# Kernel tuning notes

Measured on AMD Instinct MI355X. Metric: run time of the kernel, lower is better.

## Reference

```python
import jax, jax.numpy as jnp
import numpy as np

DIM = 1024
NUM_HEADS = 16


def setup_inputs() -> dict:
    key = jax.random.key(0)
    ks = jax.random.split(key, 7)
    B, N, C = 2, 2048, DIM
    s = 1.0 / np.sqrt(C)
    x = jax.random.normal(ks[0], (B, N, C), dtype=jnp.float32)
    Wq = jax.random.normal(ks[1], (C, C), dtype=jnp.float32) * s
    Wk = jax.random.normal(ks[2], (C, C), dtype=jnp.float32) * s
    Wv = jax.random.normal(ks[3], (C, C), dtype=jnp.float32) * s
    bq = jnp.zeros((C,), dtype=jnp.float32)
    bk = jnp.zeros((C,), dtype=jnp.float32)
    bv = jnp.zeros((C,), dtype=jnp.float32)
    return {"x": x, "Wq": Wq, "bq": bq, "Wk": Wk, "bk": bk, "Wv": Wv, "bv": bv}


def reference(x, Wq, bq, Wk, bk, Wv, bv):
    B, N, C = x.shape
    H = NUM_HEADS
    D = C // H
    # Linear projections (torch Linear: x @ W.T + b)
    q = (x @ Wq.T + bq).reshape(B, N, H, D).transpose(0, 2, 1, 3)  # [B,H,N,D]
    k = (x @ Wk.T + bk).reshape(B, N, H, D).transpose(0, 2, 1, 3)
    v = (x @ Wv.T + bv).reshape(B, N, H, D).transpose(0, 2, 1, 3)
    # NOTE: original scales by sqrt(dim)=sqrt(C), not sqrt(head_dim)
    scale = 1.0 / np.sqrt(C).astype(np.float32)
    logits = jnp.einsum('bhnd,bhmd->bhnm', q, k) * scale  # [B,H,N,N]
    attn = jax.nn.softmax(logits, axis=-1)
    out = jnp.einsum('bhnm,bhmd->bhnd', attn, v)  # [B,H,N,D]
    return out.transpose(0, 2, 1, 3).reshape(B, N, C)
```

## Files before the change

### kernel.cpp

```cpp
#include <hip/hip_runtime.h>

typedef __attribute__((ext_vector_type(8))) short bf16x8;
typedef __attribute__((ext_vector_type(4))) float f32x4;
typedef __attribute__((ext_vector_type(16))) float f32x16;
typedef __attribute__((ext_vector_type(8))) unsigned short us8;
typedef unsigned short u16;
typedef unsigned int u32;

__device__ inline u16 f2bf(float f) {
  union { float f; unsigned u; } v; v.f = f;
  unsigned r = v.u + 0x7FFFu + ((v.u >> 16) & 1u);
  return (u16)(r >> 16);
}

__device__ inline u32 cvtpk_bf16(float lo, float hi) {
  u32 r;
  asm volatile("v_cvt_pk_bf16_f32 %0, %1, %2" : "=v"(r) : "v"(lo), "v"(hi));
  return r;
}

__device__ inline void gload_lds16(const void* g, void* l) {
  __builtin_amdgcn_global_load_lds(
      (const __attribute__((address_space(1))) void*)g,
      (__attribute__((address_space(3))) void*)l, 16, 0, 0);
}

__global__ void cvt_all(const float* __restrict__ x, const float* __restrict__ wq,
                        const float* __restrict__ wk, const float* __restrict__ wv,
                        u16* __restrict__ out) {
  int i = (blockIdx.x * blockDim.x + threadIdx.x) * 4;
  const float* src; int off;
  if (i < 4194304)      { src = x;  off = 0; }
  else if (i < 5242880) { src = wq; off = 4194304; }
  else if (i < 6291456) { src = wk; off = 5242880; }
  else                  { src = wv; off = 6291456; }
  float4 v = *reinterpret_cast<const float4*>(src + (i - off));
  ushort4 o;
  o.x = f2bf(v.x); o.y = f2bf(v.y); o.z = f2bf(v.z); o.w = f2bf(v.w);
  *reinterpret_cast<ushort4*>(out + i) = o;
}

__global__ __launch_bounds__(256, 3) void gemm_qkv(
    const u16* __restrict__ X,
    const u16* __restrict__ Wq, const u16* __restrict__ Wk, const u16* __restrict__ Wv,
    const float* __restrict__ bq, const float* __restrict__ bk, const float* __restrict__ bv,
    u16* __restrict__ Oq, u16* __restrict__ Ok, u16* __restrict__ Ov)
{
  constexpr int GK = 1024;
  __shared__ __align__(16) u16 As[128 * 64];
  __shared__ __align__(16) u16 Bs[128 * 64];

  const int z = blockIdx.z;
  const u16* W = (z == 0) ? Wq : (z == 1) ? Wk : Wv;
  const float* bias = (z == 0) ? bq : (z == 1) ? bk : bv;
  u16* O = (z == 0) ? Oq : (z == 1) ? Ok : Ov;
  const float scale = (z == 0) ? (1.4426950408889634f / 32.0f) : 1.0f;

  const int tid = threadIdx.x;
  const int lane = tid & 63, w = tid >> 6;
  const int wm = w >> 1, wn = w & 1;
  const int q = lane & 15, g = lane >> 4;
  const int bm0 = blockIdx.x * 128, bn0 = blockIdx.y * 128;

  int srow[4], sgc[4];
  #pragma unroll
  for (int i = 0; i < 4; ++i) {
    int c = i * 256 + tid;
    srow[i] = c >> 3;
    sgc[i] = (((c & 7) ^ ((c >> 3) & 7)) * 8);
  }

  f32x4 acc[4][4];
  #pragma unroll
  for (int i = 0; i < 4; ++i)
    #pragma unroll
    for (int j = 0; j < 4; ++j) acc[i][j] = (f32x4){0.f, 0.f, 0.f, 0.f};

  for (int k0 = 0; k0 < GK; k0 += 64) {
    #pragma unroll
    for (int i = 0; i < 4; ++i) {
      int c8 = (i * 256 + tid) * 8;
      gload_lds16(&X[(bm0 + srow[i]) * GK + k0 + sgc[i]], &As[c8]);
      gload_lds16(&W[(bn0 + srow[i]) * GK + k0 + sgc[i]], &Bs[c8]);
    }
    __syncthreads();

    #pragma unroll
    for (int kk = 0; kk < 2; ++kk) {
      bf16x8 af[4], bfr[4];
      #pragma unroll
      for (int mi = 0; mi < 4; ++mi) {
        int row = wm * 64 + mi * 16 + q;
        af[mi] = *reinterpret_cast<const bf16x8*>(
            &As[row * 64 + (((kk * 4 + g) ^ (row & 7)) * 8)]);
      }
      #pragma unroll
      for (int ni = 0; ni < 4; ++ni) {
        int row = wn * 64 + ni * 16 + q;
        bfr[ni] = *reinterpret_cast<const bf16x8*>(
            &Bs[row * 64 + (((kk * 4 + g) ^ (row & 7)) * 8)]);
      }
      #pragma unroll
      for (int mi = 0; mi < 4; ++mi)
        #pragma unroll
        for (int ni = 0; ni < 4; ++ni)
          acc[mi][ni] = __builtin_amdgcn_mfma_f32_16x16x32_bf16(af[mi], bfr[ni], acc[mi][ni], 0, 0, 0);
    }
    __syncthreads();
  }

  #pragma unroll
  for (int mi = 0; mi < 4; ++mi) {
    #pragma unroll
    for (int ni = 0; ni < 4; ++ni) {
      int col = bn0 + wn * 64 + ni * 16 + q;
      float bb = bias[col];
      int h = col >> 6, d = col & 63;
      #pragma unroll
      for (int r = 0; r < 4; ++r) {
        int row = bm0 + wm * 64 + mi * 16 + 4 * g + r;
        int b = row >> 11, n = row & 2047;
        float v = (acc[mi][ni][r] + bb) * scale;
        O[(((b << 4) + h) * 2048 + n) * 64 + d] = f2bf(v);
      }
    }
  }
}

__global__ __launch_bounds__(512, 4) void attn_kernel(
    const u16* __restrict__ Q, const u16* __restrict__ K, const u16* __restrict__ V,
    float* __restrict__ out)
{
  __shared__ __align__(16) u16 smem[32768];
  u16* Kbase = smem;
  u16* Vbase = smem + 16384;

  const int tid = threadIdx.x;
  const int lane = tid & 63, w = tid >> 6;
  const int half = w >> 2, w4 = w & 3;
  const int tid256 = w4 * 64 + lane;
  const int ql = lane & 31, h = lane >> 5, l7 = lane & 7;

  const int lin = blockIdx.x;
  const int xcd = lin & 7, li = lin >> 3;
  const int bh = xcd * 4 + (li >> 4);
  const int b = bh >> 4, hd = bh & 15;
  const int qrow0 = (li & 15) * 128 + w4 * 32;

  const u16* Qp = Q + (bh * 2048 + qrow0 + ql) * 64;
  const u16* Kp = K + (bh * 2048 + half * 1024) * 64;
  const u16* Vp = V + (bh * 2048 + half * 1024) * 64;

  bf16x8 qf[4];
  #pragma unroll
  for (int ks = 0; ks < 4; ++ks)
    qf[ks] = *reinterpret_cast<const bf16x8*>(Qp + 16 * ks + 8 * h);

  int krow_i[2], kcolb_i[2];
  #pragma unroll
  for (int i = 0; i < 2; ++i) {
    int c = i * 256 + tid256;
    krow_i[i] = c >> 3;
    kcolb_i[i] = 16 * ((c & 7) ^ ((c >> 3) & 7));
  }

  f32x16 o0, o1;
  #pragma unroll
  for (int i = 0; i < 16; ++i) { o0[i] = 0.0f; o1[i] = 0.0f; }
  float lsum = 0.0f;

  u16* Kh = Kbase + half * 8192;
  u16* Vh = Vbase + half * 8192;
  char* vwb = (char*)(Vh) + w4 * 1024;
  const int l2 = lane * 2;

  {
    #pragma unroll
    for (int i = 0; i < 2; ++i)
      gload_lds16((const char*)(Kp + krow_i[i] * 64) + kcolb_i[i],
                  &Kh[i * 2048 + w4 * 512]);
    us8 v0 = *reinterpret_cast<const us8*>(Vp + lane * 64 + 8 * w4);
    us8 v1 = *reinterpret_cast<const us8*>(Vp + lane * 64 + 8 * (w4 + 4));
    #pragma unroll
    for (int i = 0; i < 8; ++i) {
      *(u16*)(vwb + ((i * 144) ^ l2)) = v0[i];
      *(u16*)(vwb + 4096 + ((i * 144) ^ l2)) = v1[i];
    }
    __syncthreads();
  }

  us8 vreg0, vreg1;
  for (int t = 0; t < 16; ++t) {
    const int cur = t & 1, nxt = cur ^ 1;
    const int kb = t * 64;
    if (t < 15) {
      #pragma unroll
      for (int i = 0; i < 2; ++i)
        gload_lds16((const char*)(Kp + (kb + 64 + krow_i[i]) * 64) + kcolb_i[i],
                    &Kh[nxt * 4096 + i * 2048 + w4 * 512]);
      vreg0 = *reinterpret_cast<const us8*>(Vp + (kb + 64 + lane) * 64 + 8 * w4);
      vreg1 = *reinterpret_cast<const us8*>(Vp + (kb + 64 + lane) * 64 + 8 * (w4 + 4));
    }

    f32x16 p0, p1;
    #pragma unroll
    for (int i = 0; i < 16; ++i) { p0[i] = 0.0f; p1[i] = 0.0f; }
    const u16* kl = Kh + cur * 4096;
    __builtin_amdgcn_s_setprio(1);
    #pragma unroll
    for (int ks = 0; ks < 4; ++ks) {
      int cb = (16 * ks + 8 * h) ^ (l7 << 3);
      bf16x8 kf0 = *reinterpret_cast<const bf16x8*>(kl + ql * 64 + cb);
      p0 = __builtin_amdgcn_mfma_f32_32x32x16_bf16(kf0, qf[ks], p0, 0, 0, 0);
      bf16x8 kf1 = *reinterpret_cast<const bf16x8*>(kl + (32 + ql) * 64 + cb);
      p1 = __builtin_amdgcn_mfma_f32_32x32x16_bf16(kf1, qf[ks], p1, 0, 0, 0);
    }
    __builtin_amdgcn_s_setprio(0);

    #pragma unroll
    for (int i = 0; i < 16; ++i) {
      p0[i] = __builtin_amdgcn_exp2f(p0[i]);
      p1[i] = __builtin_amdgcn_exp2f(p1[i]);
    }
    float sa[8];
    #pragma unroll
    for (int i = 0; i < 8; ++i)
      sa[i] = (p0[i] + p0[i + 8]) + (p1[i] + p1[i + 8]);
    float rs = ((sa[0] + sa[1]) + (sa[2] + sa[3])) + ((sa[4] + sa[5]) + (sa[6] + sa[7]));
    rs += __shfl_xor(rs, 32);
    lsum += rs;

    bf16x8 pf[4];
    {
      union { u32 u[4]; bf16x8 v; } fr;
      u32 a0 = cvtpk_bf16(p0[0], p0[1]),   c0 = cvtpk_bf16(p0[2], p0[3]);
      u32 b0 = cvtpk_bf16(p0[4], p0[5]),   d0 = cvtpk_bf16(p0[6], p0[7]);
      asm volatile("v_permlane32_swap_b32 %0, %1" : "+v"(a0), "+v"(b0));
      asm volatile("v_permlane32_swap_b32 %0, %1" : "+v"(c0), "+v"(d0));
      fr.u[0] = a0; fr.u[1] = c0; fr.u[2] = b0; fr.u[3] = d0;  pf[0] = fr.v;
      u32 a1 = cvtpk_bf16(p0[8], p0[9]),   c1 = cvtpk_bf16(p0[10], p0[11]);
      u32 b1 = cvtpk_bf16(p0[12], p0[13]), d1 = cvtpk_bf16(p0[14], p0[15]);
      asm volatile("v_permlane32_swap_b32 %0, %1" : "+v"(a1), "+v"(b1));
      asm volatile("v_permlane32_swap_b32 %0, %1" : "+v"(c1), "+v"(d1));
      fr.u[0] = a1; fr.u[1] = c1; fr.u[2] = b1; fr.u[3] = d1;  pf[1] = fr.v;
      u32 a2 = cvtpk_bf16(p1[0], p1[1]),   c2 = cvtpk_bf16(p1[2], p1[3]);
      u32 b2 = cvtpk_bf16(p1[4], p1[5]),   d2 = cvtpk_bf16(p1[6], p1[7]);
      asm volatile("v_permlane32_swap_b32 %0, %1" : "+v"(a2), "+v"(b2));
      asm volatile("v_permlane32_swap_b32 %0, %1" : "+v"(c2), "+v"(d2));
      fr.u[0] = a2; fr.u[1] = c2; fr.u[2] = b2; fr.u[3] = d2;  pf[2] = fr.v;
      u32 a3 = cvtpk_bf16(p1[8], p1[9]),   c3 = cvtpk_bf16(p1[10], p1[11]);
      u32 b3 = cvtpk_bf16(p1[12], p1[13]), d3 = cvtpk_bf16(p1[14], p1[15]);
      asm volatile("v_permlane32_swap_b32 %0, %1" : "+v"(a3), "+v"(b3));
      asm volatile("v_permlane32_swap_b32 %0, %1" : "+v"(c3), "+v"(d3));
      fr.u[0] = a3; fr.u[1] = c3; fr.u[2] = b3; fr.u[3] = d3;  pf[3] = fr.v;
    }

    const u16* vl = Vh + cur * 4096;
    __builtin_amdgcn_s_setprio(1);
    #pragma unroll
    for (int f = 0; f < 4; ++f) {
      int cb = (16 * f + 8 * h) ^ (l7 << 3);
      bf16x8 vf0 = *reinterpret_cast<const bf16x8*>(vl + ql * 64 + cb);
      o0 = __builtin_amdgcn_mfma_f32_32x32x16_bf16(vf0, pf[f], o0, 0, 0, 0);
      bf16x8 vf1 = *reinterpret_cast<const bf16x8*>(vl + (32 + ql) * 64 + cb);
      o1 = __builtin_amdgcn_mfma_f32_32x32x16_bf16(vf1, pf[f], o1, 0, 0, 0);
    }
    __builtin_amdgcn_s_setprio(0);

    if (t < 15) {
      char* vw = vwb + nxt * 8192;
      #pragma unroll
      for (int i = 0; i < 8; ++i) {
        *(u16*)(vw + ((i * 144) ^ l2)) = vreg0[i];
        *(u16*)(vw + 4096 + ((i * 144) ^ l2)) = vreg1[i];
      }
    }
    __syncthreads();
  }

  float* Of = reinterpret_cast<float*>(smem);
  float* Lf = Of + 4 * 64 * 33;
  const int obase = (w4 * 64 + lane) * 33;
  if (half == 1) {
    #pragma unroll
    for (int i = 0; i < 16; ++i) { Of[obase + i] = o0[i]; Of[obase + 16 + i] = o1[i]; }
    Lf[w4 * 64 + lane] = lsum;
  }
  __syncthreads();
  if (half == 0) {
    #pragma unroll
    for (int i = 0; i < 16; ++i) { o0[i] += Of[obase + i]; o1[i] += Of[obase + 16 + i]; }
    lsum += Lf[w4 * 64 + lane];

    float r = 1.0f / lsum;
    float* op = out + ((size_t)(b * 2048 + qrow0 + ql) * 1024 + hd * 64);
    #pragma unroll
    for (int g2 = 0; g2 < 4; ++g2) {
      float4 v0, v1;
      v0.x = o0[4 * g2 + 0] * r; v0.y = o0[4 * g2 + 1] * r;
      v0.z = o0[4 * g2 + 2] * r; v0.w = o0[4 * g2 + 3] * r;
      v1.x = o1[4 * g2 + 0] * r; v1.y = o1[4 * g2 + 1] * r;
      v1.z = o1[4 * g2 + 2] * r; v1.w = o1[4 * g2 + 3] * r;
      *reinterpret_cast<float4*>(op + 8 * g2 + 4 * h)      = v0;
      *reinterpret_cast<float4*>(op + 32 + 8 * g2 + 4 * h) = v1;
    }
  }
}

extern "C" void kernel_launch(void* const* d_in, const int* in_sizes, int n_in,
                              void* d_out, int out_size, void* d_ws, size_t ws_size,
                              hipStream_t stream) {
  const float* x  = (const float*)d_in[0];
  const float* Wq = (const float*)d_in[1];
  const float* bq = (const float*)d_in[2];
  const float* Wk = (const float*)d_in[3];
  const float* bk = (const float*)d_in[4];
  const float* Wv = (const float*)d_in[5];
  const float* bv = (const float*)d_in[6];
  float* out = (float*)d_out;

  u16* ws  = (u16*)d_ws;
  u16* xb  = ws;
  u16* wqb = xb  + 4194304;
  u16* wkb = wqb + 1048576;
  u16* wvb = wkb + 1048576;
  u16* qb  = wvb + 1048576;
  u16* kb  = qb  + 4194304;
  u16* vb  = kb  + 4194304;

  cvt_all<<<7168, 256, 0, stream>>>(x, Wq, Wk, Wv, ws);

  gemm_qkv<<<dim3(32, 8, 3), 256, 0, stream>>>(xb, wqb, wkb, wvb, bq, bk, bv, qb, kb, vb);

  attn_kernel<<<512, 512, 0, stream>>>(qb, kb, vb, out);
}
```

Measured before the change: 83.22 us.

## Pre-transpose V and read K/V directly from global memory in attention

Adds a separate kernel that transposes V into a [bh, d, n] layout in the workspace, reusing the bf16 x buffer. The attention kernel drops its double-buffered LDS staging of K and V and the per-iteration barrier, and loads MFMA operand fragments straight from global memory, relying on caches. This removes LDS traffic, the swizzled scatter writes and block-wide synchronisation, but adds a kernel launch and an extra pass over V. Operand loads are no longer prefetched a tile ahead, so their latency sits on the critical path.

```diff
diff --git a/kernel.cpp b/kernel.cpp
--- a/kernel.cpp
+++ b/kernel.cpp
@@ -127,19 +127,41 @@
   }
 }
 
+__global__ __launch_bounds__(256) void vt_kernel(const u16* __restrict__ V, u16* __restrict__ Vt) {
+  __shared__ u16 T[64 * 66];
+  const int bh = blockIdx.y, n0 = blockIdx.x * 64;
+  const int tid = threadIdx.x;
+  #pragma unroll
+  for (int i = 0; i < 2; ++i) {
+    int c = i * 256 + tid;
+    int n = c >> 3, col = (c & 7) * 8;
+    us8 v = *reinterpret_cast<const us8*>(&V[(bh * 2048 + n0 + n) * 64 + col]);
+    #pragma unroll
+    for (int j = 0; j < 8; ++j) T[n * 66 + col + j] = v[j];
+  }
+  __syncthreads();
+  #pragma unroll
+  for (int i = 0; i < 2; ++i) {
+    int c = i * 256 + tid;
+    int d = c >> 3, nc = (c & 7) * 8;
+    us8 o;
+    #pragma unroll
+    for (int j = 0; j < 8; ++j) o[j] = T[(nc + j) * 66 + d];
+    *reinterpret_cast<us8*>(&Vt[(bh * 64 + d) * 2048 + n0 + nc]) = o;
+  }
+}
+
 __global__ __launch_bounds__(512, 4) void attn_kernel(
-    const u16* __restrict__ Q, const u16* __restrict__ K, const u16* __restrict__ V,
+    const u16* __restrict__ Q, const u16* __restrict__ K, const u16* __restrict__ Vt,
     float* __restrict__ out)
 {
-  __shared__ __align__(16) u16 smem[32768];
-  u16* Kbase = smem;
-  u16* Vbase = smem + 16384;
+  __shared__ float Of[4 * 64 * 33];
+  __shared__ float Lf[256];
 
   const int tid = threadIdx.x;
   const int lane = tid & 63, w = tid >> 6;
   const int half = w >> 2, w4 = w & 3;
-  const int tid256 = w4 * 64 + lane;
-  const int ql = lane & 31, h = lane >> 5, l7 = lane & 7;
+  const int ql = lane & 31, h = lane >> 5;
 
   const int lin = blockIdx.x;
   const int xcd = lin & 7, li = lin >> 3;
@@ -149,70 +171,32 @@
 
   const u16* Qp = Q + (bh * 2048 + qrow0 + ql) * 64;
   const u16* Kp = K + (bh * 2048 + half * 1024) * 64;
-  const u16* Vp = V + (bh * 2048 + half * 1024) * 64;
+  const u16* Vp = Vt + bh * 64 * 2048 + half * 1024;
 
   bf16x8 qf[4];
   #pragma unroll
   for (int ks = 0; ks < 4; ++ks)
     qf[ks] = *reinterpret_cast<const bf16x8*>(Qp + 16 * ks + 8 * h);
 
-  int krow_i[2], kcolb_i[2];
-  #pragma unroll
-  for (int i = 0; i < 2; ++i) {
-    int c = i * 256 + tid256;
-    krow_i[i] = c >> 3;
-    kcolb_i[i] = 16 * ((c & 7) ^ ((c >> 3) & 7));
-  }
-
   f32x16 o0, o1;
   #pragma unroll
   for (int i = 0; i < 16; ++i) { o0[i] = 0.0f; o1[i] = 0.0f; }
   float lsum = 0.0f;
 
-  u16* Kh = Kbase + half * 8192;
-  u16* Vh = Vbase + half * 8192;
-  char* vwb = (char*)(Vh) + w4 * 1024;
-  const int l2 = lane * 2;
-
-  {
-    #pragma unroll
-    for (int i = 0; i < 2; ++i)
-      gload_lds16((const char*)(Kp + krow_i[i] * 64) + kcolb_i[i],
-                  &Kh[i * 2048 + w4 * 512]);
-    us8 v0 = *reinterpret_cast<const us8*>(Vp + lane * 64 + 8 * w4);
-    us8 v1 = *reinterpret_cast<const us8*>(Vp + lane * 64 + 8 * (w4 + 4));
-    #pragma unroll
-    for (int i = 0; i < 8; ++i) {
-      *(u16*)(vwb + ((i * 144) ^ l2)) = v0[i];
-      *(u16*)(vwb + 4096 + ((i * 144) ^ l2)) = v1[i];
-    }
-    __syncthreads();
-  }
-
-  us8 vreg0, vreg1;
   for (int t = 0; t < 16; ++t) {
-    const int cur = t & 1, nxt = cur ^ 1;
     const int kb = t * 64;
-    if (t < 15) {
-      #pragma unroll
-      for (int i = 0; i < 2; ++i)
-        gload_lds16((const char*)(Kp + (kb + 64 + krow_i[i]) * 64) + kcolb_i[i],
-                    &Kh[nxt * 4096 + i * 2048 + w4 * 512]);
-      vreg0 = *reinterpret_cast<const us8*>(Vp + (kb + 64 + lane) * 64 + 8 * w4);
-      vreg1 = *reinterpret_cast<const us8*>(Vp + (kb + 64 + lane) * 64 + 8 * (w4 + 4));
-    }
 
     f32x16 p0, p1;
     #pragma unroll
     for (int i = 0; i < 16; ++i) { p0[i] = 0.0f; p1[i] = 0.0f; }
-    const u16* kl = Kh + cur * 4096;
+    const u16* kp0 = Kp + (kb + ql) * 64 + 8 * h;
+    const u16* kp1 = Kp + (kb + 32 + ql) * 64 + 8 * h;
     __builtin_amdgcn_s_setprio(1);
     #pragma unroll
     for (int ks = 0; ks < 4; ++ks) {
-      int cb = (16 * ks + 8 * h) ^ (l7 << 3);
-      bf16x8 kf0 = *reinterpret_cast<const bf16x8*>(kl + ql * 64 + cb);
+      bf16x8 kf0 = *reinterpret_cast<const bf16x8*>(kp0 + 16 * ks);
       p0 = __builtin_amdgcn_mfma_f32_32x32x16_bf16(kf0, qf[ks], p0, 0, 0, 0);
-      bf16x8 kf1 = *reinterpret_cast<const bf16x8*>(kl + (32 + ql) * 64 + cb);
+      bf16x8 kf1 = *reinterpret_cast<const bf16x8*>(kp1 + 16 * ks);
       p1 = __builtin_amdgcn_mfma_f32_32x32x16_bf16(kf1, qf[ks], p1, 0, 0, 0);
     }
     __builtin_amdgcn_s_setprio(0);
@@ -255,31 +239,19 @@
       fr.u[0] = a3; fr.u[1] = c3; fr.u[2] = b3; fr.u[3] = d3;  pf[3] = fr.v;
     }
 
-    const u16* vl = Vh + cur * 4096;
+    const u16* vp0 = Vp + ql * 2048 + kb + 8 * h;
+    const u16* vp1 = Vp + (32 + ql) * 2048 + kb + 8 * h;
     __builtin_amdgcn_s_setprio(1);
     #pragma unroll
     for (int f = 0; f < 4; ++f) {
-      int cb = (16 * f + 8 * h) ^ (l7 << 3);
-      bf16x8 vf0 = *reinterpret_cast<const bf16x8*>(vl + ql * 64 + cb);
+      bf16x8 vf0 = *reinterpret_cast<const bf16x8*>(vp0 + 16 * f);
       o0 = __builtin_amdgcn_mfma_f32_32x32x16_bf16(vf0, pf[f], o0, 0, 0, 0);
-      bf16x8 vf1 = *reinterpret_cast<const bf16x8*>(vl + (32 + ql) * 64 + cb);
+      bf16x8 vf1 = *reinterpret_cast<const bf16x8*>(vp1 + 16 * f);
       o1 = __builtin_amdgcn_mfma_f32_32x32x16_bf16(vf1, pf[f], o1, 0, 0, 0);
     }
     __builtin_amdgcn_s_setprio(0);
-
-    if (t < 15) {
-      char* vw = vwb + nxt * 8192;
-      #pragma unroll
-      for (int i = 0; i < 8; ++i) {
-        *(u16*)(vw + ((i * 144) ^ l2)) = vreg0[i];
-        *(u16*)(vw + 4096 + ((i * 144) ^ l2)) = vreg1[i];
-      }
-    }
-    __syncthreads();
-  }
-
-  float* Of = reinterpret_cast<float*>(smem);
-  float* Lf = Of + 4 * 64 * 33;
+  }
+
   const int obase = (w4 * 64 + lane) * 33;
   if (half == 1) {
     #pragma unroll
@@ -327,10 +299,13 @@
   u16* qb  = wvb + 1048576;
   u16* kb  = qb  + 4194304;
   u16* vb  = kb  + 4194304;
+  u16* vt  = xb;
 
   cvt_all<<<7168, 256, 0, stream>>>(x, Wq, Wk, Wv, ws);
 
   gemm_qkv<<<dim3(32, 8, 3), 256, 0, stream>>>(xb, wqb, wkb, wvb, bq, bk, bv, qb, kb, vb);
 
-  attn_kernel<<<512, 512, 0, stream>>>(qb, kb, vb, out);
-}
+  vt_kernel<<<dim3(32, 32), 256, 0, stream>>>(vb, vt);
+
+  attn_kernel<<<512, 512, 0, stream>>>(qb, kb, vt, out);
+}
```

Measured after the change: 161.7 us. +94.3%, slower.

## Pre-transpose V into a separate kernel and stream it with async LDS loads

Applied to the files above, without the earlier changes.

Adds a small kernel that transposes V from [bh,n,d] to [bh,d,n] into the reused x workspace. The attention kernel then loads V tiles with direct global-to-LDS loads instead of register loads followed by scattered 2-byte LDS stores each iteration. This removes per-iteration VGPR staging and many narrow LDS writes from the attention loop. The cost is an extra launch and a full read/write pass over V.

```diff
diff --git a/kernel.cpp b/kernel.cpp
--- a/kernel.cpp
+++ b/kernel.cpp
@@ -127,8 +127,32 @@
   }
 }
 
+__global__ __launch_bounds__(256) void vt_kernel(const u16* __restrict__ V, u16* __restrict__ Vt) {
+  __shared__ u16 T[64 * 66];
+  const int bh = blockIdx.y, n0 = blockIdx.x * 64;
+  const int tid = threadIdx.x;
+  #pragma unroll
+  for (int i = 0; i < 2; ++i) {
+    int c = i * 256 + tid;
+    int n = c >> 3, col = (c & 7) * 8;
+    us8 v = *reinterpret_cast<const us8*>(&V[(bh * 2048 + n0 + n) * 64 + col]);
+    #pragma unroll
+    for (int j = 0; j < 8; ++j) T[n * 66 + col + j] = v[j];
+  }
+  __syncthreads();
+  #pragma unroll
+  for (int i = 0; i < 2; ++i) {
+    int c = i * 256 + tid;
+    int d = c >> 3, nc = (c & 7) * 8;
+    us8 o;
+    #pragma unroll
+    for (int j = 0; j < 8; ++j) o[j] = T[(nc + j) * 66 + d];
+    *reinterpret_cast<us8*>(&Vt[(bh * 64 + d) * 2048 + n0 + nc]) = o;
+  }
+}
+
 __global__ __launch_bounds__(512, 4) void attn_kernel(
-    const u16* __restrict__ Q, const u16* __restrict__ K, const u16* __restrict__ V,
+    const u16* __restrict__ Q, const u16* __restrict__ K, const u16* __restrict__ Vt,
     float* __restrict__ out)
 {
   __shared__ __align__(16) u16 smem[32768];
@@ -149,7 +173,7 @@
 
   const u16* Qp = Q + (bh * 2048 + qrow0 + ql) * 64;
   const u16* Kp = K + (bh * 2048 + half * 1024) * 64;
-  const u16* Vp = V + (bh * 2048 + half * 1024) * 64;
+  const u16* Vp = Vt + bh * 64 * 2048 + half * 1024;
 
   bf16x8 qf[4];
   #pragma unroll
@@ -171,35 +195,30 @@
 
   u16* Kh = Kbase + half * 8192;
   u16* Vh = Vbase + half * 8192;
-  char* vwb = (char*)(Vh) + w4 * 1024;
-  const int l2 = lane * 2;
 
   {
     #pragma unroll
-    for (int i = 0; i < 2; ++i)
+    for (int i = 0; i < 2; ++i) {
       gload_lds16((const char*)(Kp + krow_i[i] * 64) + kcolb_i[i],
                   &Kh[i * 2048 + w4 * 512]);
-    us8 v0 = *reinterpret_cast<const us8*>(Vp + lane * 64 + 8 * w4);
-    us8 v1 = *reinterpret_cast<const us8*>(Vp + lane * 64 + 8 * (w4 + 4));
-    #pragma unroll
-    for (int i = 0; i < 8; ++i) {
-      *(u16*)(vwb + ((i * 144) ^ l2)) = v0[i];
-      *(u16*)(vwb + 4096 + ((i * 144) ^ l2)) = v1[i];
+      gload_lds16((const char*)(Vp + krow_i[i] * 2048) + kcolb_i[i],
+                  &Vh[i * 2048 + w4 * 512]);
     }
     __syncthreads();
   }
 
-  us8 vreg0, vreg1;
   for (int t = 0; t < 16; ++t) {
     const int cur = t & 1, nxt = cur ^ 1;
     const int kb = t * 64;
     if (t < 15) {
-      #pragma unroll
-      for (int i = 0; i < 2; ++i)
-        gload_lds16((const char*)(Kp + (kb + 64 + krow_i[i]) * 64) + kcolb_i[i],
+      const int kbn = kb + 64;
+      #pragma unroll
+      for (int i = 0; i < 2; ++i) {
+        gload_lds16((const char*)(Kp + (kbn + krow_i[i]) * 64) + kcolb_i[i],
                     &Kh[nxt * 4096 + i * 2048 + w4 * 512]);
-      vreg0 = *reinterpret_cast<const us8*>(Vp + (kb + 64 + lane) * 64 + 8 * w4);
-      vreg1 = *reinterpret_cast<const us8*>(Vp + (kb + 64 + lane) * 64 + 8 * (w4 + 4));
+        gload_lds16((const char*)(Vp + krow_i[i] * 2048 + kbn) + kcolb_i[i],
+                    &Vh[nxt * 4096 + i * 2048 + w4 * 512]);
+      }
     }
 
     f32x16 p0, p1;
@@ -267,14 +286,6 @@
     }
     __builtin_amdgcn_s_setprio(0);
 
-    if (t < 15) {
-      char* vw = vwb + nxt * 8192;
-      #pragma unroll
-      for (int i = 0; i < 8; ++i) {
-        *(u16*)(vw + ((i * 144) ^ l2)) = vreg0[i];
-        *(u16*)(vw + 4096 + ((i * 144) ^ l2)) = vreg1[i];
-      }
-    }
     __syncthreads();
   }
 
@@ -327,10 +338,13 @@
   u16* qb  = wvb + 1048576;
   u16* kb  = qb  + 4194304;
   u16* vb  = kb  + 4194304;
+  u16* vt  = xb;
 
   cvt_all<<<7168, 256, 0, stream>>>(x, Wq, Wk, Wv, ws);
 
   gemm_qkv<<<dim3(32, 8, 3), 256, 0, stream>>>(xb, wqb, wkb, wvb, bq, bk, bv, qb, kb, vb);
 
-  attn_kernel<<<512, 512, 0, stream>>>(qb, kb, vb, out);
-}
+  vt_kernel<<<dim3(32, 32), 256, 0, stream>>>(vb, vt);
+
+  attn_kernel<<<512, 512, 0, stream>>>(qb, kb, vt, out);
+}
```

Measured after the change: 85.28 us. 1.02x slower.
